# Kernel optimization log

Hardware: AMD Instinct MI355X
Metric: run time of the kernel (lower is better)

The kernel has to match this reference:

```python
import jax, jax.numpy as jnp
import numpy as np

NUM_NODES = 100000
OUT_CHANNELS = 64
NUM_EDGES = 3200000


def setup_inputs() -> dict:
    key = jax.random.key(0)
    k1, k2, k3 = jax.random.split(key, 3)
    edge_index = jax.random.randint(k1, (2, NUM_EDGES), 0, NUM_NODES, dtype=jnp.int64) if jax.config.jax_enable_x64 else jax.random.randint(k1, (2, NUM_EDGES), 0, NUM_NODES, dtype=jnp.int32)
    # nn.Linear default init: U(-1/sqrt(fan_in), 1/sqrt(fan_in)); use randn-scale for a correctness baseline
    W_weight = jax.random.normal(k2, (OUT_CHANNELS, NUM_NODES), dtype=jnp.float32) * (1.0 / np.sqrt(NUM_NODES))
    W_bias = jax.random.normal(k3, (OUT_CHANNELS,), dtype=jnp.float32) * (1.0 / np.sqrt(NUM_NODES))
    return {"edge_index": edge_index, "W_weight": W_weight, "W_bias": W_bias}


def reference(edge_index, W_weight, W_bias):
    # A is the [N, N] binary COO adjacency (duplicate edges sum, matching
    # an uncoalesced torch sparse COO matmul). logits = A @ W_weight.T + b.
    num_nodes = W_weight.shape[1]
    row = edge_index[0] - jnp.min(edge_index[0])  # row = row - row.min()
    col = edge_index[1]
    Wt = W_weight.T  # [N, C]
    # SpMM as gather + segment-sum: logits[i] = sum_{(i,j) in E} Wt[j]
    logits = jax.ops.segment_sum(Wt[col], row, num_segments=num_nodes)  # [N, C]
    logits = logits + W_bias
    return jax.nn.log_softmax(logits, axis=1)
```

## Files before the change

kernel.cpp:

```cpp
#include <hip/hip_runtime.h>
#include <hip/hip_bf16.h>
#include <limits.h>

#define NUM_NODES 100000
#define OUT_CH 64
#define NUM_EDGES 3200000
#define BROWS 128
#define NBUCK 782
#define NPBLK 256
#define EPB (NUM_EDGES / NPBLK)
#define I4PB (EPB / 4)
#define STAGECAP 6144

__global__ __launch_bounds__(256) void LINK_62689342652831_min_kernel(
    const int* __restrict__ rows, int* __restrict__ minp) {
    int tid = blockIdx.x * 256 + threadIdx.x;
    int stride = gridDim.x * 256;
    const int4* r4 = (const int4*)rows;
    int m = INT_MAX;
    for (int i = tid; i < NUM_EDGES / 4; i += stride) {
        int4 v = r4[i];
        m = min(m, min(min(v.x, v.y), min(v.z, v.w)));
    }
    for (int off = 32; off > 0; off >>= 1) m = min(m, __shfl_xor(m, off, 64));
    __shared__ int sm[4];
    if ((threadIdx.x & 63) == 0) sm[threadIdx.x >> 6] = m;
    __syncthreads();
    if (threadIdx.x == 0) {
        int mm = min(min(sm[0], sm[1]), min(sm[2], sm[3]));
        atomicMin(minp, mm);
    }
}

__global__ void LINK_62689342652831_transpose_kernel(const float* __restrict__ W,
                                                     unsigned short* __restrict__ Wtb) {
    __shared__ float tile[64][65];
    int n0 = blockIdx.x * 64;
    int tx = threadIdx.x & 63;
    int ty = threadIdx.x >> 6;
    for (int c = ty; c < 64; c += 4) {
        int n = n0 + tx;
        tile[c][tx] = (n < NUM_NODES) ? W[(size_t)c * NUM_NODES + n] : 0.0f;
    }
    __syncthreads();
    for (int i = ty; i < 64; i += 4) {
        int n = n0 + i;
        if (n < NUM_NODES) {
            __hip_bfloat16 bv = __float2bfloat16(tile[tx][i]);
            Wtb[(size_t)n * OUT_CH + tx] = *(unsigned short*)&bv;
        }
    }
}

__global__ __launch_bounds__(512) void LINK_62689342652831_hist2d_kernel(
    const int* __restrict__ rows, const int* __restrict__ minp,
    int* __restrict__ hist2d) {
    __shared__ int h[NBUCK];
    for (int i = threadIdx.x; i < NBUCK; i += 512) h[i] = 0;
    __syncthreads();
    int minv = *minp;
    int blk = blockIdx.x;
    const int4* r4 = (const int4*)rows;
    for (int i = threadIdx.x; i < I4PB; i += 512) {
        int4 v = r4[blk * I4PB + i];
        atomicAdd(&h[(unsigned)(v.x - minv) >> 7], 1);
        atomicAdd(&h[(unsigned)(v.y - minv) >> 7], 1);
        atomicAdd(&h[(unsigned)(v.z - minv) >> 7], 1);
        atomicAdd(&h[(unsigned)(v.w - minv) >> 7], 1);
    }
    __syncthreads();
    for (int i = threadIdx.x; i < NBUCK; i += 512) hist2d[blk * NBUCK + i] = h[i];
}

__global__ __launch_bounds__(512) void LINK_62689342652831_colscan_kernel(
    int* __restrict__ hist2d, int* __restrict__ totals) {
    int lane = threadIdx.x & 63;
    int wid = threadIdx.x >> 6;
    int b = blockIdx.x * 8 + wid;
    if (b >= NBUCK) return;
    int carry = 0;
    for (int rnd = 0; rnd < NPBLK / 64; ++rnd) {
        int blk = rnd * 64 + lane;
        int v = hist2d[blk * NBUCK + b];
        int x = v;
        for (int off = 1; off < 64; off <<= 1) {
            int y = __shfl_up(x, off, 64);
            if (lane >= off) x += y;
        }
        hist2d[blk * NBUCK + b] = x - v + carry;
        carry += __shfl(x, 63, 64);
    }
    if (lane == 0) totals[b] = carry;
}

__global__ __launch_bounds__(1024) void LINK_62689342652831_bscan_kernel(
    const int* __restrict__ totals, int* __restrict__ bstart) {
    __shared__ int ss[1024];
    int t = threadIdx.x;
    int v = (t < NBUCK) ? totals[t] : 0;
    ss[t] = v;
    __syncthreads();
    for (int off = 1; off < 1024; off <<= 1) {
        int x = (t >= off) ? ss[t - off] : 0;
        __syncthreads();
        ss[t] += x;
        __syncthreads();
    }
    if (t < NBUCK) bstart[t] = ss[t] - v;
    if (t == NBUCK - 1) bstart[NBUCK] = ss[t];
}

__global__ __launch_bounds__(512) void LINK_62689342652831_part_kernel(
    const int* __restrict__ rows, const int* __restrict__ cols,
    const int* __restrict__ minp, const int* __restrict__ hist2d,
    const int* __restrict__ bstart, unsigned int* __restrict__ packed) {
    __shared__ int offs_l[NBUCK];
    __shared__ int lcur[NBUCK];
    int blk = blockIdx.x;
    for (int i = threadIdx.x; i < NBUCK; i += 512) {
        offs_l[i] = bstart[i] + hist2d[blk * NBUCK + i];
        lcur[i] = 0;
    }
    __syncthreads();
    int minv = *minp;
    const int4* r4 = (const int4*)rows;
    const int4* c4 = (const int4*)cols;
    for (int i = threadIdx.x; i < I4PB; i += 512) {
        int4 rv = r4[blk * I4PB + i];
        int4 cv = c4[blk * I4PB + i];
#pragma unroll
        for (int k = 0; k < 4; ++k) {
            int r = ((k == 0) ? rv.x : (k == 1) ? rv.y : (k == 2) ? rv.z : rv.w) - minv;
            int c = (k == 0) ? cv.x : (k == 1) ? cv.y : (k == 2) ? cv.z : cv.w;
            int b = (unsigned)r >> 7;
            int pos = offs_l[b] + atomicAdd(&lcur[b], 1);
            packed[pos] = ((unsigned)(r & (BROWS - 1)) << 17) | (unsigned)c;
        }
    }
}

__global__ __launch_bounds__(512) void LINK_62689342652831_spmm_kernel(
    const unsigned int* __restrict__ packed, const int* __restrict__ bstart,
    const unsigned short* __restrict__ Wtb, const float* __restrict__ bias,
    float* __restrict__ out) {
    __shared__ unsigned int sh[8192];
    __shared__ int rhist[BROWS];
    __shared__ int rstart[BROWS + 1];
    __shared__ int rcur[BROWS];
    unsigned int* sorted = sh;

    int lane = threadIdx.x & 63;
    int wid = threadIdx.x >> 6;
    int b = blockIdx.x;
    int s = bstart[b], e = bstart[b + 1];
    int n = e - s;

    if (n <= STAGECAP) {
        if (threadIdx.x < BROWS) rhist[threadIdx.x] = 0;
        __syncthreads();
        for (int i = threadIdx.x; i < n; i += 512)
            atomicAdd(&rhist[packed[s + i] >> 17], 1);
        __syncthreads();
        if (wid == 0) {
            int c0 = rhist[lane], c1 = rhist[lane + 64];
            int x0 = c0, x1 = c1;
            for (int off = 1; off < 64; off <<= 1) {
                int y0 = __shfl_up(x0, off, 64);
                int y1 = __shfl_up(x1, off, 64);
                if (lane >= off) { x0 += y0; x1 += y1; }
            }
            int t0 = __shfl(x0, 63, 64);
            rstart[lane] = x0 - c0;
            rstart[lane + 64] = x1 - c1 + t0;
            rcur[lane] = x0 - c0;
            rcur[lane + 64] = x1 - c1 + t0;
            if (lane == 63) rstart[128] = x1 + t0;
        }
        __syncthreads();
        for (int i = threadIdx.x; i < n; i += 512) {
            unsigned int u = packed[s + i];
            int pos = atomicAdd(&rcur[u >> 17], 1);
            sorted[pos] = u;
        }
        __syncthreads();

        const uint2* Wt2 = (const uint2*)Wtb;
        int q = lane >> 4;
        int ql = lane & 15;
        float b0 = bias[4 * ql], b1 = bias[4 * ql + 1],
              b2 = bias[4 * ql + 2], b3 = bias[4 * ql + 3];

        for (int r = wid; r < BROWS; r += 8) {
            int gr = b * BROWS + r;
            if (gr >= NUM_NODES) continue;
            int s0 = rstart[r], e0 = rstart[r + 1];
            float a0 = 0, a1 = 0, a2 = 0, a3 = 0;
            int i = s0 + q;
            for (; i + 4 < e0; i += 8) {
                unsigned int ua = sorted[i], ub = sorted[i + 4];
                uint2 wa = Wt2[(size_t)(ua & 0x1FFFF) * 16 + ql];
                uint2 wb = Wt2[(size_t)(ub & 0x1FFFF) * 16 + ql];
                a0 += __uint_as_float(wa.x << 16);
                a1 += __uint_as_float(wa.x & 0xFFFF0000u);
                a2 += __uint_as_float(wa.y << 16);
                a3 += __uint_as_float(wa.y & 0xFFFF0000u);
                a0 += __uint_as_float(wb.x << 16);
                a1 += __uint_as_float(wb.x & 0xFFFF0000u);
                a2 += __uint_as_float(wb.y << 16);
                a3 += __uint_as_float(wb.y & 0xFFFF0000u);
            }
            for (; i < e0; i += 4) {
                unsigned int u = sorted[i];
                uint2 w = Wt2[(size_t)(u & 0x1FFFF) * 16 + ql];
                a0 += __uint_as_float(w.x << 16);
                a1 += __uint_as_float(w.x & 0xFFFF0000u);
                a2 += __uint_as_float(w.y << 16);
                a3 += __uint_as_float(w.y & 0xFFFF0000u);
            }
            a0 += __shfl_xor(a0, 32, 64); a1 += __shfl_xor(a1, 32, 64);
            a2 += __shfl_xor(a2, 32, 64); a3 += __shfl_xor(a3, 32, 64);
            a0 += __shfl_xor(a0, 16, 64); a1 += __shfl_xor(a1, 16, 64);
            a2 += __shfl_xor(a2, 16, 64); a3 += __shfl_xor(a3, 16, 64);

            float x0 = a0 + b0, x1 = a1 + b1, x2 = a2 + b2, x3 = a3 + b3;
            float m = fmaxf(fmaxf(x0, x1), fmaxf(x2, x3));
            for (int off = 8; off > 0; off >>= 1) m = fmaxf(m, __shfl_xor(m, off, 64));
            float ssum = expf(x0 - m) + expf(x1 - m) + expf(x2 - m) + expf(x3 - m);
            for (int off = 8; off > 0; off >>= 1) ssum += __shfl_xor(ssum, off, 64);
            float l = m + logf(ssum);
            if (lane < 16) {
                float4 o = {x0 - l, x1 - l, x2 - l, x3 - l};
                *(float4*)&out[(size_t)gr * OUT_CH + 4 * ql] = o;
            }
        }
    } else {
        float* acc = (float*)sh;
        for (int i = threadIdx.x; i < BROWS * OUT_CH; i += 512) acc[i] = 0.0f;
        __syncthreads();
        for (int i = s + wid; i < e; i += 8) {
            unsigned int u = packed[i];
            float v = __uint_as_float((unsigned int)Wtb[(size_t)(u & 0x1FFFF) * OUT_CH + lane] << 16);
            atomicAdd(&acc[(u >> 17) * OUT_CH + lane], v);
        }
        __syncthreads();
        float bsv = bias[lane];
        for (int r = wid; r < BROWS; r += 8) {
            int gr = b * BROWS + r;
            if (gr >= NUM_NODES) continue;
            float x = acc[r * OUT_CH + lane] + bsv;
            float m = x;
            for (int off = 32; off > 0; off >>= 1) m = fmaxf(m, __shfl_xor(m, off, 64));
            float ex = expf(x - m);
            float ssum = ex;
            for (int off = 32; off > 0; off >>= 1) ssum += __shfl_xor(ssum, off, 64);
            out[(size_t)gr * OUT_CH + lane] = x - m - logf(ssum);
        }
    }
}

__global__ void LINK_62689342652831_minf_kernel(const int* __restrict__ rows, int n,
                                                int* __restrict__ minp) {
    int tid = blockIdx.x * blockDim.x + threadIdx.x;
    int stride = gridDim.x * blockDim.x;
    int m = INT_MAX;
    for (int i = tid; i < n; i += stride) m = min(m, rows[i]);
    for (int off = 32; off > 0; off >>= 1) m = min(m, __shfl_xor(m, off, 64));
    if ((threadIdx.x & 63) == 0) atomicMin(minp, m);
}

__global__ void LINK_62689342652831_scatter_kernel(const int* __restrict__ rows,
                                                   const int* __restrict__ cols,
                                                   const float* __restrict__ W,
                                                   const int* __restrict__ minp,
                                                   float* __restrict__ out) {
    int lane = threadIdx.x & 63;
    int gw = (blockIdx.x * blockDim.x + threadIdx.x) >> 6;
    int nw = (gridDim.x * blockDim.x) >> 6;
    int minv = *minp;
    for (int e = gw; e < NUM_EDGES; e += nw) {
        int r = rows[e] - minv;
        int c = cols[e];
        float v = W[(size_t)lane * NUM_NODES + c];
        unsafeAtomicAdd(&out[(size_t)r * 64 + lane], v);
    }
}

__global__ void LINK_62689342652831_logsoftmax_kernel(float* __restrict__ out,
                                                      const float* __restrict__ bias) {
    int lane = threadIdx.x & 63;
    int gw = (blockIdx.x * blockDim.x + threadIdx.x) >> 6;
    int nw = (gridDim.x * blockDim.x) >> 6;
    float b = bias[lane];
    for (int r = gw; r < NUM_NODES; r += nw) {
        float x = out[(size_t)r * 64 + lane] + b;
        float m = x;
        for (int off = 32; off > 0; off >>= 1) m = fmaxf(m, __shfl_xor(m, off, 64));
        float e = expf(x - m);
        float s = e;
        for (int off = 32; off > 0; off >>= 1) s += __shfl_xor(s, off, 64);
        out[(size_t)r * 64 + lane] = x - m - logf(s);
    }
}

extern "C" void kernel_launch(void* const* d_in, const int* in_sizes, int n_in,
                              void* d_out, int out_size, void* d_ws, size_t ws_size,
                              hipStream_t stream) {
    const int* edges = (const int*)d_in[0];
    const int* rows = edges;
    const int* cols = edges + NUM_EDGES;
    const float* W = (const float*)d_in[1];
    const float* bias = (const float*)d_in[2];
    float* out = (float*)d_out;

    char* ws = (char*)d_ws;
    const size_t OFF_MIN = 0;
    const size_t OFF_BSTART = 256;
    const size_t OFF_TOT = 4096;
    const size_t OFF_H2D = 8192;
    const size_t OFF_PACKED = 1024 * 1024;
    const size_t OFF_WTB = OFF_PACKED + (size_t)NUM_EDGES * 4;
    const size_t need = OFF_WTB + (size_t)NUM_NODES * OUT_CH * 2;

    int* minp = (int*)(ws + OFF_MIN);
    int* bstart = (int*)(ws + OFF_BSTART);
    int* totals = (int*)(ws + OFF_TOT);
    int* hist2d = (int*)(ws + OFF_H2D);
    unsigned int* packed = (unsigned int*)(ws + OFF_PACKED);
    unsigned short* Wtb = (unsigned short*)(ws + OFF_WTB);

    hipMemsetAsync(minp, 0x7f, sizeof(int), stream);

    if (ws_size >= need) {
        LINK_62689342652831_min_kernel<<<256, 256, 0, stream>>>(rows, minp);
        LINK_62689342652831_transpose_kernel<<<(NUM_NODES + 63) / 64, 256, 0, stream>>>(W, Wtb);
        LINK_62689342652831_hist2d_kernel<<<NPBLK, 512, 0, stream>>>(rows, minp, hist2d);
        LINK_62689342652831_colscan_kernel<<<(NBUCK + 7) / 8, 512, 0, stream>>>(hist2d, totals);
        LINK_62689342652831_bscan_kernel<<<1, 1024, 0, stream>>>(totals, bstart);
        LINK_62689342652831_part_kernel<<<NPBLK, 512, 0, stream>>>(rows, cols, minp, hist2d,
                                                                   bstart, packed);
        LINK_62689342652831_spmm_kernel<<<NBUCK, 512, 0, stream>>>(packed, bstart, Wtb,
                                                                   bias, out);
    } else {
        LINK_62689342652831_minf_kernel<<<2048, 256, 0, stream>>>(rows, NUM_EDGES, minp);
        hipMemsetAsync(d_out, 0, (size_t)out_size * sizeof(float), stream);
        LINK_62689342652831_scatter_kernel<<<2048, 256, 0, stream>>>(rows, cols, W, minp, out);
        LINK_62689342652831_logsoftmax_kernel<<<4096, 256, 0, stream>>>(out, bias);
    }
}
```

Before: 132.6 us.

## Fuse min and transpose kernels, cache packed edges in registers, widen SpMM gathers

Merges the row-min reduction and the W transpose into one launch, using disjoint block ranges, so one kernel launch and its tail disappear. In the SpMM staging path, each thread keeps its up to 12 packed edges in registers, so the counting-sort scatter no longer re-reads them from global memory. The gather now uses 8 lanes per edge with 16-byte uint4 loads instead of 16 lanes with 8-byte loads, which halves the lanes per row and shortens the reductions. In exchange, the kernel uses more registers per thread, which can lower occupancy.

```diff
diff --git a/kernel.cpp b/kernel.cpp
--- a/kernel.cpp
+++ b/kernel.cpp
@@ -11,43 +11,45 @@
 #define EPB (NUM_EDGES / NPBLK)
 #define I4PB (EPB / 4)
 #define STAGECAP 6144
-
-__global__ __launch_bounds__(256) void LINK_62689342652831_min_kernel(
+#define NTRANS 1563
+
+__global__ __launch_bounds__(256) void LINK_62689342652831_mintrans_kernel(
+    const float* __restrict__ W, unsigned short* __restrict__ Wtb,
     const int* __restrict__ rows, int* __restrict__ minp) {
-    int tid = blockIdx.x * 256 + threadIdx.x;
-    int stride = gridDim.x * 256;
-    const int4* r4 = (const int4*)rows;
-    int m = INT_MAX;
-    for (int i = tid; i < NUM_EDGES / 4; i += stride) {
-        int4 v = r4[i];
-        m = min(m, min(min(v.x, v.y), min(v.z, v.w)));
-    }
-    for (int off = 32; off > 0; off >>= 1) m = min(m, __shfl_xor(m, off, 64));
-    __shared__ int sm[4];
-    if ((threadIdx.x & 63) == 0) sm[threadIdx.x >> 6] = m;
-    __syncthreads();
-    if (threadIdx.x == 0) {
-        int mm = min(min(sm[0], sm[1]), min(sm[2], sm[3]));
-        atomicMin(minp, mm);
-    }
-}
-
-__global__ void LINK_62689342652831_transpose_kernel(const float* __restrict__ W,
-                                                     unsigned short* __restrict__ Wtb) {
     __shared__ float tile[64][65];
-    int n0 = blockIdx.x * 64;
-    int tx = threadIdx.x & 63;
-    int ty = threadIdx.x >> 6;
-    for (int c = ty; c < 64; c += 4) {
-        int n = n0 + tx;
-        tile[c][tx] = (n < NUM_NODES) ? W[(size_t)c * NUM_NODES + n] : 0.0f;
-    }
-    __syncthreads();
-    for (int i = ty; i < 64; i += 4) {
-        int n = n0 + i;
-        if (n < NUM_NODES) {
-            __hip_bfloat16 bv = __float2bfloat16(tile[tx][i]);
-            Wtb[(size_t)n * OUT_CH + tx] = *(unsigned short*)&bv;
+    if (blockIdx.x < NTRANS) {
+        int n0 = blockIdx.x * 64;
+        int tx = threadIdx.x & 63;
+        int ty = threadIdx.x >> 6;
+        for (int c = ty; c < 64; c += 4) {
+            int n = n0 + tx;
+            tile[c][tx] = (n < NUM_NODES) ? W[(size_t)c * NUM_NODES + n] : 0.0f;
+        }
+        __syncthreads();
+        for (int i = ty; i < 64; i += 4) {
+            int n = n0 + i;
+            if (n < NUM_NODES) {
+                __hip_bfloat16 bv = __float2bfloat16(tile[tx][i]);
+                Wtb[(size_t)n * OUT_CH + tx] = *(unsigned short*)&bv;
+            }
+        }
+    } else {
+        int blk = blockIdx.x - NTRANS;
+        int tid = blk * 256 + threadIdx.x;
+        int stride = 256 * 256;
+        const int4* r4 = (const int4*)rows;
+        int m = INT_MAX;
+        for (int i = tid; i < NUM_EDGES / 4; i += stride) {
+            int4 v = r4[i];
+            m = min(m, min(min(v.x, v.y), min(v.z, v.w)));
+        }
+        for (int off = 32; off > 0; off >>= 1) m = min(m, __shfl_xor(m, off, 64));
+        int* sm = (int*)tile;
+        if ((threadIdx.x & 63) == 0) sm[threadIdx.x >> 6] = m;
+        __syncthreads();
+        if (threadIdx.x == 0) {
+            int mm = min(min(sm[0], sm[1]), min(sm[2], sm[3]));
+            atomicMin(minp, mm);
         }
     }
 }
@@ -156,10 +158,18 @@
     int n = e - s;
 
     if (n <= STAGECAP) {
+        unsigned int pk[12];
         if (threadIdx.x < BROWS) rhist[threadIdx.x] = 0;
         __syncthreads();
-        for (int i = threadIdx.x; i < n; i += 512)
-            atomicAdd(&rhist[packed[s + i] >> 17], 1);
+#pragma unroll
+        for (int k = 0; k < 12; ++k) {
+            int idx = threadIdx.x + k * 512;
+            pk[k] = 0u;
+            if (idx < n) {
+                pk[k] = packed[s + idx];
+                atomicAdd(&rhist[pk[k] >> 17], 1);
+            }
+        }
         __syncthreads();
         if (wid == 0) {
             int c0 = rhist[lane], c1 = rhist[lane + 64];
@@ -177,60 +187,82 @@
             if (lane == 63) rstart[128] = x1 + t0;
         }
         __syncthreads();
-        for (int i = threadIdx.x; i < n; i += 512) {
-            unsigned int u = packed[s + i];
-            int pos = atomicAdd(&rcur[u >> 17], 1);
-            sorted[pos] = u;
-        }
-        __syncthreads();
-
-        const uint2* Wt2 = (const uint2*)Wtb;
-        int q = lane >> 4;
-        int ql = lane & 15;
-        float b0 = bias[4 * ql], b1 = bias[4 * ql + 1],
-              b2 = bias[4 * ql + 2], b3 = bias[4 * ql + 3];
+#pragma unroll
+        for (int k = 0; k < 12; ++k) {
+            int idx = threadIdx.x + k * 512;
+            if (idx < n) {
+                int pos = atomicAdd(&rcur[pk[k] >> 17], 1);
+                sorted[pos] = pk[k];
+            }
+        }
+        __syncthreads();
+
+        const uint4* Wt4 = (const uint4*)Wtb;
+        int g = lane >> 3;
+        int gl = lane & 7;
+        float4 bA = *(const float4*)&bias[8 * gl];
+        float4 bB = *(const float4*)&bias[8 * gl + 4];
 
         for (int r = wid; r < BROWS; r += 8) {
             int gr = b * BROWS + r;
             if (gr >= NUM_NODES) continue;
             int s0 = rstart[r], e0 = rstart[r + 1];
-            float a0 = 0, a1 = 0, a2 = 0, a3 = 0;
-            int i = s0 + q;
-            for (; i + 4 < e0; i += 8) {
-                unsigned int ua = sorted[i], ub = sorted[i + 4];
-                uint2 wa = Wt2[(size_t)(ua & 0x1FFFF) * 16 + ql];
-                uint2 wb = Wt2[(size_t)(ub & 0x1FFFF) * 16 + ql];
+            float a0 = 0, a1 = 0, a2 = 0, a3 = 0, a4 = 0, a5 = 0, a6 = 0, a7 = 0;
+            int i = s0 + g;
+            for (; i + 8 < e0; i += 16) {
+                unsigned int ua = sorted[i], ub = sorted[i + 8];
+                uint4 wa = Wt4[(ua & 0x1FFFF) * 8 + gl];
+                uint4 wb = Wt4[(ub & 0x1FFFF) * 8 + gl];
                 a0 += __uint_as_float(wa.x << 16);
                 a1 += __uint_as_float(wa.x & 0xFFFF0000u);
                 a2 += __uint_as_float(wa.y << 16);
                 a3 += __uint_as_float(wa.y & 0xFFFF0000u);
+                a4 += __uint_as_float(wa.z << 16);
+                a5 += __uint_as_float(wa.z & 0xFFFF0000u);
+                a6 += __uint_as_float(wa.w << 16);
+                a7 += __uint_as_float(wa.w & 0xFFFF0000u);
                 a0 += __uint_as_float(wb.x << 16);
                 a1 += __uint_as_float(wb.x & 0xFFFF0000u);
                 a2 += __uint_as_float(wb.y << 16);
                 a3 += __uint_as_float(wb.y & 0xFFFF0000u);
-            }
-            for (; i < e0; i += 4) {
+                a4 += __uint_as_float(wb.z << 16);
+                a5 += __uint_as_float(wb.z & 0xFFFF0000u);
+                a6 += __uint_as_float(wb.w << 16);
+                a7 += __uint_as_float(wb.w & 0xFFFF0000u);
+            }
+            for (; i < e0; i += 8) {
                 unsigned int u = sorted[i];
-                uint2 w = Wt2[(size_t)(u & 0x1FFFF) * 16 + ql];
+                uint4 w = Wt4[(u & 0x1FFFF) * 8 + gl];
                 a0 += __uint_as_float(w.x << 16);
                 a1 += __uint_as_float(w.x & 0xFFFF0000u);
                 a2 += __uint_as_float(w.y << 16);
                 a3 += __uint_as_float(w.y & 0xFFFF0000u);
-            }
-            a0 += __shfl_xor(a0, 32, 64); a1 += __shfl_xor(a1, 32, 64);
-            a2 += __shfl_xor(a2, 32, 64); a3 += __shfl_xor(a3, 32, 64);
-            a0 += __shfl_xor(a0, 16, 64); a1 += __shfl_xor(a1, 16, 64);
-            a2 += __shfl_xor(a2, 16, 64); a3 += __shfl_xor(a3, 16, 64);
-
-            float x0 = a0 + b0, x1 = a1 + b1, x2 = a2 + b2, x3 = a3 + b3;
-            float m = fmaxf(fmaxf(x0, x1), fmaxf(x2, x3));
-            for (int off = 8; off > 0; off >>= 1) m = fmaxf(m, __shfl_xor(m, off, 64));
-            float ssum = expf(x0 - m) + expf(x1 - m) + expf(x2 - m) + expf(x3 - m);
-            for (int off = 8; off > 0; off >>= 1) ssum += __shfl_xor(ssum, off, 64);
+                a4 += __uint_as_float(w.z << 16);
+                a5 += __uint_as_float(w.z & 0xFFFF0000u);
+                a6 += __uint_as_float(w.w << 16);
+                a7 += __uint_as_float(w.w & 0xFFFF0000u);
+            }
+#pragma unroll
+            for (int off = 8; off <= 32; off <<= 1) {
+                a0 += __shfl_xor(a0, off, 64); a1 += __shfl_xor(a1, off, 64);
+                a2 += __shfl_xor(a2, off, 64); a3 += __shfl_xor(a3, off, 64);
+                a4 += __shfl_xor(a4, off, 64); a5 += __shfl_xor(a5, off, 64);
+                a6 += __shfl_xor(a6, off, 64); a7 += __shfl_xor(a7, off, 64);
+            }
+            float x0 = a0 + bA.x, x1 = a1 + bA.y, x2 = a2 + bA.z, x3 = a3 + bA.w;
+            float x4 = a4 + bB.x, x5 = a5 + bB.y, x6 = a6 + bB.z, x7 = a7 + bB.w;
+            float m = fmaxf(fmaxf(fmaxf(x0, x1), fmaxf(x2, x3)),
+                            fmaxf(fmaxf(x4, x5), fmaxf(x6, x7)));
+            for (int off = 1; off <= 4; off <<= 1) m = fmaxf(m, __shfl_xor(m, off, 64));
+            float ssum = expf(x0 - m) + expf(x1 - m) + expf(x2 - m) + expf(x3 - m) +
+                         expf(x4 - m) + expf(x5 - m) + expf(x6 - m) + expf(x7 - m);
+            for (int off = 1; off <= 4; off <<= 1) ssum += __shfl_xor(ssum, off, 64);
             float l = m + logf(ssum);
-            if (lane < 16) {
-                float4 o = {x0 - l, x1 - l, x2 - l, x3 - l};
-                *(float4*)&out[(size_t)gr * OUT_CH + 4 * ql] = o;
+            if (g == 0) {
+                float4 oA = {x0 - l, x1 - l, x2 - l, x3 - l};
+                float4 oB = {x4 - l, x5 - l, x6 - l, x7 - l};
+                *(float4*)&out[(size_t)gr * OUT_CH + 8 * gl] = oA;
+                *(float4*)&out[(size_t)gr * OUT_CH + 8 * gl + 4] = oB;
             }
         }
     } else {
@@ -331,8 +363,7 @@
     hipMemsetAsync(minp, 0x7f, sizeof(int), stream);
 
     if (ws_size >= need) {
-        LINK_62689342652831_min_kernel<<<256, 256, 0, stream>>>(rows, minp);
-        LINK_62689342652831_transpose_kernel<<<(NUM_NODES + 63) / 64, 256, 0, stream>>>(W, Wtb);
+        LINK_62689342652831_mintrans_kernel<<<NTRANS + 256, 256, 0, stream>>>(W, Wtb, rows, minp);
         LINK_62689342652831_hist2d_kernel<<<NPBLK, 512, 0, stream>>>(rows, minp, hist2d);
         LINK_62689342652831_colscan_kernel<<<(NBUCK + 7) / 8, 512, 0, stream>>>(hist2d, totals);
         LINK_62689342652831_bscan_kernel<<<1, 1024, 0, stream>>>(totals, bstart);
```

Result: slower. 138.1 us (+4.1%).

## Halve row buckets, shrink SpMM blocks, and fuse min-reduce with transpose

Applied to the files above, without the earlier changes.

Row buckets drop from 128 to 64 rows, which doubles the bucket count to 1563 and lets each SpMM block use 256 threads and a smaller shared staging buffer, so more blocks fit per CU. The min-reduction and the W transpose are merged into one launch so the two independent jobs share a grid and one launch is saved. The bucket scan now handles two entries per thread to cover the larger bucket count. The risks are a larger hist2d and part/colscan overhead, and the fallback path running more often if buckets exceed the smaller STAGECAP.

```diff
diff --git a/kernel.cpp b/kernel.cpp
--- a/kernel.cpp
+++ b/kernel.cpp
@@ -5,49 +5,52 @@
 #define NUM_NODES 100000
 #define OUT_CH 64
 #define NUM_EDGES 3200000
-#define BROWS 128
-#define NBUCK 782
+#define BROWS 64
+#define BSHIFT 6
+#define NBUCK 1563
 #define NPBLK 256
 #define EPB (NUM_EDGES / NPBLK)
 #define I4PB (EPB / 4)
-#define STAGECAP 6144
-
-__global__ __launch_bounds__(256) void LINK_62689342652831_min_kernel(
+#define STAGECAP 4096
+#define NTRANS 1563
+
+__global__ __launch_bounds__(256) void LINK_62689342652831_mintrans_kernel(
+    const float* __restrict__ W, unsigned short* __restrict__ Wtb,
     const int* __restrict__ rows, int* __restrict__ minp) {
-    int tid = blockIdx.x * 256 + threadIdx.x;
-    int stride = gridDim.x * 256;
-    const int4* r4 = (const int4*)rows;
-    int m = INT_MAX;
-    for (int i = tid; i < NUM_EDGES / 4; i += stride) {
-        int4 v = r4[i];
-        m = min(m, min(min(v.x, v.y), min(v.z, v.w)));
-    }
-    for (int off = 32; off > 0; off >>= 1) m = min(m, __shfl_xor(m, off, 64));
-    __shared__ int sm[4];
-    if ((threadIdx.x & 63) == 0) sm[threadIdx.x >> 6] = m;
-    __syncthreads();
-    if (threadIdx.x == 0) {
-        int mm = min(min(sm[0], sm[1]), min(sm[2], sm[3]));
-        atomicMin(minp, mm);
-    }
-}
-
-__global__ void LINK_62689342652831_transpose_kernel(const float* __restrict__ W,
-                                                     unsigned short* __restrict__ Wtb) {
     __shared__ float tile[64][65];
-    int n0 = blockIdx.x * 64;
-    int tx = threadIdx.x & 63;
-    int ty = threadIdx.x >> 6;
-    for (int c = ty; c < 64; c += 4) {
-        int n = n0 + tx;
-        tile[c][tx] = (n < NUM_NODES) ? W[(size_t)c * NUM_NODES + n] : 0.0f;
-    }
-    __syncthreads();
-    for (int i = ty; i < 64; i += 4) {
-        int n = n0 + i;
-        if (n < NUM_NODES) {
-            __hip_bfloat16 bv = __float2bfloat16(tile[tx][i]);
-            Wtb[(size_t)n * OUT_CH + tx] = *(unsigned short*)&bv;
+    if (blockIdx.x < NTRANS) {
+        int n0 = blockIdx.x * 64;
+        int tx = threadIdx.x & 63;
+        int ty = threadIdx.x >> 6;
+        for (int c = ty; c < 64; c += 4) {
+            int n = n0 + tx;
+            tile[c][tx] = (n < NUM_NODES) ? W[(size_t)c * NUM_NODES + n] : 0.0f;
+        }
+        __syncthreads();
+        for (int i = ty; i < 64; i += 4) {
+            int n = n0 + i;
+            if (n < NUM_NODES) {
+                __hip_bfloat16 bv = __float2bfloat16(tile[tx][i]);
+                Wtb[(size_t)n * OUT_CH + tx] = *(unsigned short*)&bv;
+            }
+        }
+    } else {
+        int blk = blockIdx.x - NTRANS;
+        int tid = blk * 256 + threadIdx.x;
+        int stride = 256 * 256;
+        const int4* r4 = (const int4*)rows;
+        int m = INT_MAX;
+        for (int i = tid; i < NUM_EDGES / 4; i += stride) {
+            int4 v = r4[i];
+            m = min(m, min(min(v.x, v.y), min(v.z, v.w)));
+        }
+        for (int off = 32; off > 0; off >>= 1) m = min(m, __shfl_xor(m, off, 64));
+        int* sm = (int*)tile;
+        if ((threadIdx.x & 63) == 0) sm[threadIdx.x >> 6] = m;
+        __syncthreads();
+        if (threadIdx.x == 0) {
+            int mm = min(min(sm[0], sm[1]), min(sm[2], sm[3]));
+            atomicMin(minp, mm);
         }
     }
 }
@@ -63,10 +66,10 @@
     const int4* r4 = (const int4*)rows;
     for (int i = threadIdx.x; i < I4PB; i += 512) {
         int4 v = r4[blk * I4PB + i];
-        atomicAdd(&h[(unsigned)(v.x - minv) >> 7], 1);
-        atomicAdd(&h[(unsigned)(v.y - minv) >> 7], 1);
-        atomicAdd(&h[(unsigned)(v.z - minv) >> 7], 1);
-        atomicAdd(&h[(unsigned)(v.w - minv) >> 7], 1);
+        atomicAdd(&h[(unsigned)(v.x - minv) >> BSHIFT], 1);
+        atomicAdd(&h[(unsigned)(v.y - minv) >> BSHIFT], 1);
+        atomicAdd(&h[(unsigned)(v.z - minv) >> BSHIFT], 1);
+        atomicAdd(&h[(unsigned)(v.w - minv) >> BSHIFT], 1);
     }
     __syncthreads();
     for (int i = threadIdx.x; i < NBUCK; i += 512) hist2d[blk * NBUCK + i] = h[i];
@@ -97,8 +100,11 @@
     const int* __restrict__ totals, int* __restrict__ bstart) {
     __shared__ int ss[1024];
     int t = threadIdx.x;
-    int v = (t < NBUCK) ? totals[t] : 0;
-    ss[t] = v;
+    int i0 = 2 * t, i1 = 2 * t + 1;
+    int v0 = (i0 < NBUCK) ? totals[i0] : 0;
+    int v1 = (i1 < NBUCK) ? totals[i1] : 0;
+    int p1 = v0 + v1;
+    ss[t] = p1;
     __syncthreads();
     for (int off = 1; off < 1024; off <<= 1) {
         int x = (t >= off) ? ss[t - off] : 0;
@@ -106,8 +112,10 @@
         ss[t] += x;
         __syncthreads();
     }
-    if (t < NBUCK) bstart[t] = ss[t] - v;
-    if (t == NBUCK - 1) bstart[NBUCK] = ss[t];
+    int texcl = ss[t] - p1;
+    if (i0 < NBUCK) bstart[i0] = texcl;
+    if (i1 < NBUCK) bstart[i1] = texcl + v0;
+    if (t == 1023) bstart[NBUCK] = ss[1023];
 }
 
 __global__ __launch_bounds__(512) void LINK_62689342652831_part_kernel(
@@ -132,22 +140,21 @@
         for (int k = 0; k < 4; ++k) {
             int r = ((k == 0) ? rv.x : (k == 1) ? rv.y : (k == 2) ? rv.z : rv.w) - minv;
             int c = (k == 0) ? cv.x : (k == 1) ? cv.y : (k == 2) ? cv.z : cv.w;
-            int b = (unsigned)r >> 7;
+            int b = (unsigned)r >> BSHIFT;
             int pos = offs_l[b] + atomicAdd(&lcur[b], 1);
             packed[pos] = ((unsigned)(r & (BROWS - 1)) << 17) | (unsigned)c;
         }
     }
 }
 
-__global__ __launch_bounds__(512) void LINK_62689342652831_spmm_kernel(
+__global__ __launch_bounds__(256) void LINK_62689342652831_spmm_kernel(
     const unsigned int* __restrict__ packed, const int* __restrict__ bstart,
     const unsigned short* __restrict__ Wtb, const float* __restrict__ bias,
     float* __restrict__ out) {
-    __shared__ unsigned int sh[8192];
+    __shared__ unsigned int sorted[STAGECAP];
     __shared__ int rhist[BROWS];
     __shared__ int rstart[BROWS + 1];
     __shared__ int rcur[BROWS];
-    unsigned int* sorted = sh;
 
     int lane = threadIdx.x & 63;
     int wid = threadIdx.x >> 6;
@@ -158,26 +165,22 @@
     if (n <= STAGECAP) {
         if (threadIdx.x < BROWS) rhist[threadIdx.x] = 0;
         __syncthreads();
-        for (int i = threadIdx.x; i < n; i += 512)
+        for (int i = threadIdx.x; i < n; i += 256)
             atomicAdd(&rhist[packed[s + i] >> 17], 1);
         __syncthreads();
-        if (wid == 0) {
-            int c0 = rhist[lane], c1 = rhist[lane + 64];
-            int x0 = c0, x1 = c1;
+        if (threadIdx.x < 64) {
+            int c0 = rhist[lane];
+            int x0 = c0;
             for (int off = 1; off < 64; off <<= 1) {
                 int y0 = __shfl_up(x0, off, 64);
-                int y1 = __shfl_up(x1, off, 64);
-                if (lane >= off) { x0 += y0; x1 += y1; }
-            }
-            int t0 = __shfl(x0, 63, 64);
+                if (lane >= off) x0 += y0;
+            }
             rstart[lane] = x0 - c0;
-            rstart[lane + 64] = x1 - c1 + t0;
             rcur[lane] = x0 - c0;
-            rcur[lane + 64] = x1 - c1 + t0;
-            if (lane == 63) rstart[128] = x1 + t0;
-        }
-        __syncthreads();
-        for (int i = threadIdx.x; i < n; i += 512) {
+            if (lane == 63) rstart[64] = x0;
+        }
+        __syncthreads();
+        for (int i = threadIdx.x; i < n; i += 256) {
             unsigned int u = packed[s + i];
             int pos = atomicAdd(&rcur[u >> 17], 1);
             sorted[pos] = u;
@@ -190,7 +193,7 @@
         float b0 = bias[4 * ql], b1 = bias[4 * ql + 1],
               b2 = bias[4 * ql + 2], b3 = bias[4 * ql + 3];
 
-        for (int r = wid; r < BROWS; r += 8) {
+        for (int r = wid; r < BROWS; r += 4) {
             int gr = b * BROWS + r;
             if (gr >= NUM_NODES) continue;
             int s0 = rstart[r], e0 = rstart[r + 1];
@@ -234,17 +237,17 @@
             }
         }
     } else {
-        float* acc = (float*)sh;
-        for (int i = threadIdx.x; i < BROWS * OUT_CH; i += 512) acc[i] = 0.0f;
-        __syncthreads();
-        for (int i = s + wid; i < e; i += 8) {
+        float* acc = (float*)sorted;
+        for (int i = threadIdx.x; i < BROWS * OUT_CH; i += 256) acc[i] = 0.0f;
+        __syncthreads();
+        for (int i = s + wid; i < e; i += 4) {
             unsigned int u = packed[i];
             float v = __uint_as_float((unsigned int)Wtb[(size_t)(u & 0x1FFFF) * OUT_CH + lane] << 16);
             atomicAdd(&acc[(u >> 17) * OUT_CH + lane], v);
         }
         __syncthreads();
         float bsv = bias[lane];
-        for (int r = wid; r < BROWS; r += 8) {
+        for (int r = wid; r < BROWS; r += 4) {
             int gr = b * BROWS + r;
             if (gr >= NUM_NODES) continue;
             float x = acc[r * OUT_CH + lane] + bsv;
@@ -315,9 +318,9 @@
     char* ws = (char*)d_ws;
     const size_t OFF_MIN = 0;
     const size_t OFF_BSTART = 256;
-    const size_t OFF_TOT = 4096;
-    const size_t OFF_H2D = 8192;
-    const size_t OFF_PACKED = 1024 * 1024;
+    const size_t OFF_TOT = 8192;
+    const size_t OFF_H2D = 16384;
+    const size_t OFF_PACKED = 2 * 1024 * 1024;
     const size_t OFF_WTB = OFF_PACKED + (size_t)NUM_EDGES * 4;
     const size_t need = OFF_WTB + (size_t)NUM_NODES * OUT_CH * 2;
 
@@ -331,14 +334,13 @@
     hipMemsetAsync(minp, 0x7f, sizeof(int), stream);
 
     if (ws_size >= need) {
-        LINK_62689342652831_min_kernel<<<256, 256, 0, stream>>>(rows, minp);
-        LINK_62689342652831_transpose_kernel<<<(NUM_NODES + 63) / 64, 256, 0, stream>>>(W, Wtb);
+        LINK_62689342652831_mintrans_kernel<<<NTRANS + 256, 256, 0, stream>>>(W, Wtb, rows, minp);
         LINK_62689342652831_hist2d_kernel<<<NPBLK, 512, 0, stream>>>(rows, minp, hist2d);
         LINK_62689342652831_colscan_kernel<<<(NBUCK + 7) / 8, 512, 0, stream>>>(hist2d, totals);
         LINK_62689342652831_bscan_kernel<<<1, 1024, 0, stream>>>(totals, bstart);
         LINK_62689342652831_part_kernel<<<NPBLK, 512, 0, stream>>>(rows, cols, minp, hist2d,
                                                                    bstart, packed);
-        LINK_62689342652831_spmm_kernel<<<NBUCK, 512, 0, stream>>>(packed, bstart, Wtb,
+        LINK_62689342652831_spmm_kernel<<<NBUCK, 256, 0, stream>>>(packed, bstart, Wtb,
                                                                    bias, out);
     } else {
         LINK_62689342652831_minf_kernel<<<2048, 256, 0, stream>>>(rows, NUM_EDGES, minp);
```

Measured after the change: 136.9 us. +3.2%, slower.
